# Kernel tuning notes

Hardware: AMD Instinct MI355X
Metric: run time of the kernel (lower is better)

Reference implementation:

```python
import jax, jax.numpy as jnp
import numpy as np

N, E, D_IN, D_OUT = 100000, 1250000, 64, 100


def setup_inputs() -> dict:
    key = jax.random.key(0)
    ks = jax.random.split(key, 12)
    inp = {
        "x": jax.random.normal(ks[0], (N, D_IN), dtype=jnp.float32),
        "edge_index": jax.random.randint(ks[1], (2, E), 0, N, dtype=jnp.int64),
        "edge_weight": jax.random.uniform(ks[2], (E,), dtype=jnp.float32),
        # ChebConv(64,100,K=1): one weight + bias
        "W10": jax.random.normal(ks[3], (D_IN, D_OUT), dtype=jnp.float32) * 0.1,
        "b1": jnp.zeros((D_OUT,), dtype=jnp.float32),
        # ChebConv(64,100,K=2)
        "W20": jax.random.normal(ks[4], (D_IN, D_OUT), dtype=jnp.float32) * 0.1,
        "W21": jax.random.normal(ks[5], (D_IN, D_OUT), dtype=jnp.float32) * 0.1,
        "b2": jnp.zeros((D_OUT,), dtype=jnp.float32),
        # ChebConv(64,100,K=3)
        "W30": jax.random.normal(ks[6], (D_IN, D_OUT), dtype=jnp.float32) * 0.1,
        "W31": jax.random.normal(ks[7], (D_IN, D_OUT), dtype=jnp.float32) * 0.1,
        "W32": jax.random.normal(ks[8], (D_IN, D_OUT), dtype=jnp.float32) * 0.1,
        "b3": jnp.zeros((D_OUT,), dtype=jnp.float32),
    }
    return inp


def _cheb_norm(edge_index, edge_weight, n):
    # PyG ChebConv.__norm__ with normalization='sym', lambda_max=2.0:
    # L_hat = (2/lambda_max) * (I - D^-1/2 A D^-1/2) - I = -D^-1/2 A D^-1/2
    # (the +1 diagonal of L and the -1 self-loop cancel), diag entries are 0.
    row, col = edge_index[0], edge_index[1]
    deg = jax.ops.segment_sum(edge_weight, row, num_segments=n)
    dis = jnp.where(deg > 0, jax.lax.rsqrt(jnp.where(deg > 0, deg, 1.0)), 0.0)
    return -dis[row] * edge_weight * dis[col]


def _cheb_conv(x, edge_index, w_hat, weights, bias):
    # out = sum_k T_k(L_hat) x @ W_k + b, with T0=x, T1=Lx, T_k=2L T_{k-1}-T_{k-2}
    n = x.shape[0]
    row, col = edge_index[0], edge_index[1]

    def prop(t):  # L_hat @ t via edge gather/scatter
        return jax.ops.segment_sum(t[row] * w_hat[:, None], col, num_segments=n)

    tx0 = x
    out = tx0 @ weights[0]
    if len(weights) > 1:
        tx1 = prop(tx0)
        out = out + tx1 @ weights[1]
        for k in range(2, len(weights)):
            tx2 = 2.0 * prop(tx1) - tx0
            out = out + tx2 @ weights[k]
            tx0, tx1 = tx1, tx2
    return out + bias


def reference(x, edge_index, edge_weight, W10, b1, W20, W21, b2, W30, W31, W32, b3):
    w_hat = _cheb_norm(edge_index, edge_weight, x.shape[0])
    s1 = _cheb_conv(x, edge_index, w_hat, [W10], b1)
    s2 = _cheb_conv(x, edge_index, w_hat, [W20, W21], b2)
    s3 = _cheb_conv(x, edge_index, w_hat, [W30, W31, W32], b3)
    return jnp.concatenate([s1, s2, s3], axis=1)  # [N, 300]
```

## Files before the change

### kernel.cpp

```cpp
#include <hip/hip_runtime.h>


typedef __attribute__((ext_vector_type(8))) short short8;
typedef __attribute__((ext_vector_type(8))) unsigned short ushort8;
typedef __attribute__((ext_vector_type(4))) float f32x4;

#define CAPB 8192
#define MAXBUCK 512

__device__ inline float bf2f(unsigned short u) {
    return __uint_as_float(((unsigned int)u) << 16);
}
__device__ inline unsigned short f2bf(float f) {
    unsigned int u = __float_as_uint(f);
    u = (u + 0x7FFF + ((u >> 16) & 1)) >> 16;
    return (unsigned short)u;
}

__global__ __launch_bounds__(256) void part_kernel(
        const int* __restrict__ row, const int* __restrict__ col,
        const float* __restrict__ ew, int* __restrict__ colcur,
        int* __restrict__ rowcur, uint2* __restrict__ colpart,
        uint2* __restrict__ rowpart, int E, int nbuck, int chunk) {
    __shared__ int hc[MAXBUCK];
    __shared__ int hr[MAXBUCK];
    const int t = threadIdx.x;
    const int s = blockIdx.x * chunk;
    const int e = min(E, s + chunk);
    if (s >= E) return;
    for (int i = t; i < nbuck; i += 256) { hc[i] = 0; hr[i] = 0; }
    __syncthreads();
    for (int i = s + t; i < e; i += 256) {
        atomicAdd(&hc[col[i] >> 8], 1);
        atomicAdd(&hr[row[i] >> 8], 1);
    }
    __syncthreads();
    for (int i = t; i < nbuck; i += 256) {
        int n = hc[i];
        hc[i] = n ? atomicAdd(&colcur[i], n) : 0;
        n = hr[i];
        hr[i] = n ? atomicAdd(&rowcur[i], n) : 0;
    }
    __syncthreads();
    for (int i = s + t; i < e; i += 256) {
        int r = row[i], c = col[i];
        float w = ew[i];
        int cb = c >> 8, rb = r >> 8;
        int pc = atomicAdd(&hc[cb], 1);
        if (pc < CAPB)
            colpart[(size_t)cb * CAPB + pc] =
                make_uint2(((unsigned)(c & 255) << 24) | (unsigned)r, __float_as_uint(w));
        int pr = atomicAdd(&hr[rb], 1);
        if (pr < CAPB)
            rowpart[(size_t)rb * CAPB + pr] = make_uint2((unsigned)r, __float_as_uint(w));
    }
}

__global__ __launch_bounds__(256) void fine_row_kernel(
        const int* __restrict__ rowcur, const uint2* __restrict__ rowpart,
        float* __restrict__ dis, int N) {
    __shared__ float s[256];
    const int b = blockIdx.x, t = threadIdx.x;
    const int sz = min(rowcur[b], CAPB);
    const uint2* part = rowpart + (size_t)b * CAPB;
    s[t] = 0.f;
    __syncthreads();
    for (int i = t; i < sz; i += 256) {
        uint2 rec = part[i];
        atomicAdd(&s[rec.x & 255u], __uint_as_float(rec.y));
    }
    __syncthreads();
    int r = (b << 8) + t;
    if (r < N) {
        float d = s[t];
        dis[r] = (d > 0.f) ? rsqrtf(d) : 0.f;
    }
}

__global__ void colbase_scan_kernel(const int* __restrict__ colcur,
                                    int* __restrict__ colbase,
                                    int* __restrict__ rowptr, int N, int nbuck) {
    __shared__ int s[MAXBUCK];
    int t = threadIdx.x;
    int v = (t < nbuck) ? min(colcur[t], CAPB) : 0;
    s[t] = v;
    __syncthreads();
    for (int o = 1; o < MAXBUCK; o <<= 1) {
        int u = (t >= o) ? s[t - o] : 0;
        __syncthreads();
        s[t] += u;
        __syncthreads();
    }
    if (t < nbuck) colbase[t] = s[t] - v;
    if (t == MAXBUCK - 1) rowptr[N] = s[MAXBUCK - 1];
}

__global__ __launch_bounds__(256) void fine_col_kernel(
        const int* __restrict__ colcur, const int* __restrict__ colbase,
        const uint2* __restrict__ colpart, const float* __restrict__ dis,
        uint2* __restrict__ erec, int* __restrict__ rowptr, int N) {
    __shared__ int h[256];
    __shared__ int sc[256];
    __shared__ int cur[256];
    const int b = blockIdx.x, t = threadIdx.x;
    const int sz = min(colcur[b], CAPB);
    const uint2* part = colpart + (size_t)b * CAPB;
    h[t] = 0;
    __syncthreads();
    for (int i = t; i < sz; i += 256) atomicAdd(&h[part[i].x >> 24], 1);
    __syncthreads();
    int v = h[t];
    sc[t] = v;
    __syncthreads();
    for (int o = 1; o < 256; o <<= 1) {
        int u = (t >= o) ? sc[t - o] : 0;
        __syncthreads();
        sc[t] += u;
        __syncthreads();
    }
    int excl = sc[t] - v;
    const int base = colbase[b];
    int c = (b << 8) + t;
    if (c < N) rowptr[c] = base + excl;
    cur[t] = excl;
    __syncthreads();
    for (int i = t; i < sz; i += 256) {
        uint2 rec = part[i];
        int coff = rec.x >> 24;
        int r = rec.x & 0xFFFFFFu;
        int pos = atomicAdd(&cur[coff], 1);
        float wd = __uint_as_float(rec.y) * dis[r];
        erec[(size_t)base + pos] = make_uint2((unsigned)r, __float_as_uint(wd));
    }
}

__global__ void deg_count_kernel(const int* __restrict__ row, const int* __restrict__ col,
                                 const float* __restrict__ ew,
                                 float* __restrict__ deg, int* __restrict__ cnt, int E) {
    int e = blockIdx.x * 256 + threadIdx.x;
    if (e < E) {
        atomicAdd(&deg[row[e]], ew[e]);
        atomicAdd(&cnt[col[e]], 1);
    }
}

__global__ void scan1_kernel(const int* __restrict__ cnt, int* __restrict__ pre,
                             int* __restrict__ bsum, int N) {
    __shared__ int s[256];
    int t = threadIdx.x;
    int i = blockIdx.x * 256 + t;
    int v = (i < N) ? cnt[i] : 0;
    s[t] = v;
    __syncthreads();
    for (int o = 1; o < 256; o <<= 1) {
        int u = (t >= o) ? s[t - o] : 0;
        __syncthreads();
        s[t] += u;
        __syncthreads();
    }
    if (i < N) pre[i] = s[t] - v;
    if (t == 255) bsum[blockIdx.x] = s[255];
}

__global__ void scan2_kernel(const int* __restrict__ bsum, int* __restrict__ bpre, int nb) {
    __shared__ int s[512];
    int t = threadIdx.x;
    int v = (t < nb) ? bsum[t] : 0;
    s[t] = v;
    __syncthreads();
    for (int o = 1; o < 512; o <<= 1) {
        int u = (t >= o) ? s[t - o] : 0;
        __syncthreads();
        s[t] += u;
        __syncthreads();
    }
    if (t < nb) bpre[t] = s[t] - v;
}

__global__ void scan3_kernel(int* __restrict__ rowptr, int* __restrict__ cursor,
                             const int* __restrict__ bpre, int N, int E) {
    int i = blockIdx.x * 256 + threadIdx.x;
    if (i < N) {
        int v = rowptr[i] + bpre[i >> 8];
        rowptr[i] = v;
        cursor[i] = v;
    }
    if (i == 0) rowptr[N] = E;
}

__global__ void scatter_compact_kernel(const int* __restrict__ row, const int* __restrict__ col,
                                       const float* __restrict__ ew, int* __restrict__ cursor,
                                       uint2* __restrict__ erec, int E) {
    int e = blockIdx.x * 256 + threadIdx.x;
    if (e < E) {
        int p = atomicAdd(&cursor[col[e]], 1);
        erec[p] = make_uint2((unsigned)row[e], __float_as_uint(ew[e]));
    }
}

__global__ void cvt_dis_kernel(const float* __restrict__ x, unsigned short* __restrict__ xb,
                               const float* __restrict__ deg, float* __restrict__ dis,
                               int N, int total4, int dodis) {
    int i = blockIdx.x * 256 + threadIdx.x;
    if (i < total4) {
        float4 v = reinterpret_cast<const float4*>(x)[i];
        ushort4 o;
        o.x = f2bf(v.x); o.y = f2bf(v.y); o.z = f2bf(v.z); o.w = f2bf(v.w);
        reinterpret_cast<ushort4*>(xb)[i] = o;
    }
    if (dodis && i < N) {
        float d = deg[i];
        dis[i] = (d > 0.f) ? rsqrtf(d) : 0.f;
    }
}

__global__ void gather_kernel(const int* __restrict__ ptr, const uint2* __restrict__ erec,
                              const float* __restrict__ dis,
                              const unsigned short* __restrict__ src,
                              unsigned short* __restrict__ dst, int N, int premul) {
    int node = blockIdx.x * 4 + (threadIdx.x >> 6);
    int lane = threadIdx.x & 63;
    if (node >= N) return;
    int s = ptr[node];
    int d = ptr[node + 1] - s;
    float acc = 0.f;
    for (int base = 0; base < d; base += 64) {
        int n = min(64, d - base);
        int ex = 0;
        float w = 0.f;
        if (lane < n) {
            uint2 e = erec[s + base + lane];
            ex = (int)e.x;
            w = __uint_as_float(e.y);
            if (!premul) w *= dis[ex];
        }
        int n4 = (n + 3) & ~3;
        for (int j = 0; j < n4; j += 4) {
            int r0 = __shfl(ex, j + 0, 64);
            int r1 = __shfl(ex, j + 1, 64);
            int r2 = __shfl(ex, j + 2, 64);
            int r3 = __shfl(ex, j + 3, 64);
            float w0 = __shfl(w, j + 0, 64);
            float w1 = __shfl(w, j + 1, 64);
            float w2 = __shfl(w, j + 2, 64);
            float w3 = __shfl(w, j + 3, 64);
            float v0 = bf2f(src[(size_t)r0 * 64 + lane]);
            float v1 = bf2f(src[(size_t)r1 * 64 + lane]);
            float v2 = bf2f(src[(size_t)r2 * 64 + lane]);
            float v3 = bf2f(src[(size_t)r3 * 64 + lane]);
            acc = fmaf(w0, v0, acc);
            acc = fmaf(w1, v1, acc);
            acc = fmaf(w2, v2, acc);
            acc = fmaf(w3, v3, acc);
        }
    }
    dst[(size_t)node * 64 + lane] = f2bf(-dis[node] * acc);
}

__global__ void prep_w_kernel(const float* __restrict__ W10, const float* __restrict__ W20,
                              const float* __restrict__ W21, const float* __restrict__ W30,
                              const float* __restrict__ W31, const float* __restrict__ W32,
                              unsigned short* __restrict__ imgW) {
    int i = blockIdx.x * 256 + threadIdx.x;
    if (i >= 6 * 7168) return;
    int img = i / 7168;
    int rem = i - img * 7168;
    int colc = rem >> 6;
    int k = rem & 63;
    const float* W;
    switch (img) {
        case 0: W = W10; break;
        case 1: W = W20; break;
        case 2: W = W21; break;
        case 3: W = W30; break;
        case 4: W = W31; break;
        default: W = W32; break;
    }
    float v = (colc < 100) ? W[k * 100 + colc] : 0.f;
    int g = k >> 3, j = k & 7;
    imgW[img * 7168 + colc * 64 + ((g ^ (colc & 7)) << 3) + j] = f2bf(v);
}

__global__ __launch_bounds__(256) void gemm_mfma_kernel(
        const unsigned short* __restrict__ xb, const unsigned short* __restrict__ tx1b,
        const unsigned short* __restrict__ p2b, const unsigned short* __restrict__ imgW,
        const float* __restrict__ b1, const float* __restrict__ b2,
        const float* __restrict__ b3, float* __restrict__ out, int N) {
    __shared__ unsigned short Ft[64 * 64];
    __shared__ unsigned short Ws[112 * 64];
    const int bid = blockIdx.x;
    const int seg = bid % 3;
    const int tile = bid / 3;
    const int row0 = tile * 64;
    const int tid = threadIdx.x;
    const int wv = tid >> 6;
    const int l = tid & 63;
    const int m = l & 15;
    const int q = l >> 4;

    f32x4 acc[7];
#pragma unroll
    for (int t = 0; t < 7; ++t) acc[t] = (f32x4){0.f, 0.f, 0.f, 0.f};

    const int imgBase = (seg * (seg + 1) / 2) * 7168;

    for (int c = 0; c <= seg; ++c) {
        const unsigned short* __restrict__ src = (c == 0) ? xb : (c == 1) ? tx1b : p2b;
#pragma unroll
        for (int it = 0; it < 2; ++it) {
            int i = tid + it * 256;
            int r = i >> 3, g = i & 7;
            int grow = row0 + r;
            ushort8 v = {0, 0, 0, 0, 0, 0, 0, 0};
            if (grow < N) {
                v = *reinterpret_cast<const ushort8*>(src + (size_t)grow * 64 + g * 8);
                if (c == 2) {
                    ushort8 xv = *reinterpret_cast<const ushort8*>(xb + (size_t)grow * 64 + g * 8);
#pragma unroll
                    for (int jj = 0; jj < 8; ++jj)
                        v[jj] = f2bf(2.f * bf2f(v[jj]) - bf2f(xv[jj]));
                }
            }
            *reinterpret_cast<ushort8*>(&Ft[r * 64 + ((g ^ (r & 7)) << 3)]) = v;
        }
        const uint4* wsrc = reinterpret_cast<const uint4*>(imgW + imgBase + c * 7168);
        uint4* wdst = reinterpret_cast<uint4*>(Ws);
#pragma unroll
        for (int it = 0; it < 4; ++it) {
            int i = tid + it * 256;
            if (i < 896) wdst[i] = wsrc[i];
        }
        __syncthreads();

        const int arow = wv * 16 + m;
#pragma unroll
        for (int ks = 0; ks < 2; ++ks) {
            short8 a = *reinterpret_cast<const short8*>(
                &Ft[arow * 64 + (((ks * 4 + q) ^ (arow & 7)) << 3)]);
#pragma unroll
            for (int t = 0; t < 7; ++t) {
                int n = t * 16 + m;
                short8 b = *reinterpret_cast<const short8*>(
                    &Ws[n * 64 + (((ks * 4 + q) ^ (n & 7)) << 3)]);
                acc[t] = __builtin_amdgcn_mfma_f32_16x16x32_bf16(a, b, acc[t], 0, 0, 0);
            }
        }
        __syncthreads();
    }

    const float* bsel = (seg == 0) ? b1 : (seg == 1) ? b2 : b3;
#pragma unroll
    for (int t = 0; t < 7; ++t) {
        int colseg = t * 16 + m;
        if (colseg >= 100) continue;
        float bv = bsel[colseg];
#pragma unroll
        for (int i = 0; i < 4; ++i) {
            int grow = row0 + wv * 16 + q * 4 + i;
            if (grow < N) out[(size_t)grow * 300 + seg * 100 + colseg] = acc[t][i] + bv;
        }
    }
}

extern "C" void kernel_launch(void* const* d_in, const int* in_sizes, int n_in,
                              void* d_out, int out_size, void* d_ws, size_t ws_size,
                              hipStream_t stream) {
    const float* x   = (const float*)d_in[0];
    const int*   ei  = (const int*)d_in[1];
    const float* ew  = (const float*)d_in[2];
    const float* W10 = (const float*)d_in[3];
    const float* b1  = (const float*)d_in[4];
    const float* W20 = (const float*)d_in[5];
    const float* W21 = (const float*)d_in[6];
    const float* b2  = (const float*)d_in[7];
    const float* W30 = (const float*)d_in[8];
    const float* W31 = (const float*)d_in[9];
    const float* W32 = (const float*)d_in[10];
    const float* b3  = (const float*)d_in[11];
    float* out = (float*)d_out;

    const int N = in_sizes[0] / 64;
    const int E = in_sizes[2];
    const int* row = ei;
    const int* col = ei + E;
    const int nb = (N + 255) / 256;
    const int eb = (E + 255) / 256;
    const int nbuck = (N + 255) >> 8;

    int total4 = N * 16;
    int pg = (N + 3) / 4;
    int ntile = (N + 63) / 64;

    char* base = (char*)d_ws;
    size_t off = 0;
    auto alloc = [&](size_t bytes) { size_t o = off; off = (off + bytes + 15) & ~(size_t)15; return o; };

    float* dis           = (float*)(base + alloc((size_t)4 * N));
    int*   rowptr        = (int*)(base + alloc((size_t)4 * (N + 1)));
    int*   colcur        = (int*)(base + alloc((size_t)4 * MAXBUCK * 2));
    int*   rowcur        = colcur + MAXBUCK;
    int*   colbase       = (int*)(base + alloc((size_t)4 * MAXBUCK));
    unsigned short* xb   = (unsigned short*)(base + alloc((size_t)128 * N));
    unsigned short* tx1b = (unsigned short*)(base + alloc((size_t)128 * N));
    unsigned short* p2b  = (unsigned short*)(base + alloc((size_t)128 * N));
    unsigned short* imgW = (unsigned short*)(base + alloc((size_t)2 * 6 * 7168));
    uint2* erec          = (uint2*)(base + alloc((size_t)8 * E));
    size_t mainfix = off;
    uint2* colpart       = (uint2*)(base + alloc((size_t)8 * nbuck * CAPB));
    uint2* rowpart       = (uint2*)(base + alloc((size_t)8 * nbuck * CAPB));
    size_t mainneed = off;

    bool mainok = (N < (1 << 24)) && (nbuck <= MAXBUCK) && (mainneed <= ws_size);

    if (mainok) {
        const int PBLK = 512;
        int chunk = (E + PBLK - 1) / PBLK;

        hipMemsetAsync(colcur, 0, (size_t)4 * MAXBUCK * 2, stream);
        part_kernel<<<PBLK, 256, 0, stream>>>(row, col, ew, colcur, rowcur,
                                              colpart, rowpart, E, nbuck, chunk);
        fine_row_kernel<<<nbuck, 256, 0, stream>>>(rowcur, rowpart, dis, N);
        colbase_scan_kernel<<<1, MAXBUCK, 0, stream>>>(colcur, colbase, rowptr, N, nbuck);
        fine_col_kernel<<<nbuck, 256, 0, stream>>>(colcur, colbase, colpart, dis,
                                                   erec, rowptr, N);
        cvt_dis_kernel<<<(total4 + 255) / 256, 256, 0, stream>>>(x, xb, nullptr, nullptr,
                                                                 N, total4, 0);
        prep_w_kernel<<<(6 * 7168 + 255) / 256, 256, 0, stream>>>(W10, W20, W21, W30, W31, W32, imgW);

        gather_kernel<<<pg, 256, 0, stream>>>(rowptr, erec, dis, xb, tx1b, N, 1);
        gather_kernel<<<pg, 256, 0, stream>>>(rowptr, erec, dis, tx1b, p2b, N, 1);
        gemm_mfma_kernel<<<ntile * 3, 256, 0, stream>>>(xb, tx1b, p2b, imgW, b1, b2, b3, out, N);
    } else {
        off = mainfix;
        float* deg    = (float*)(base + alloc((size_t)4 * N));
        int*   cursor = (int*)(base + alloc((size_t)4 * N));
        int*   bsum   = (int*)(base + alloc((size_t)4 * nb));
        int*   bpre   = (int*)(base + alloc((size_t)4 * nb));

        hipMemsetAsync(deg, 0, (size_t)4 * N, stream);
        hipMemsetAsync(cursor, 0, (size_t)4 * N, stream);
        deg_count_kernel<<<eb, 256, 0, stream>>>(row, col, ew, deg, cursor, E);
        scan1_kernel<<<nb, 256, 0, stream>>>(cursor, rowptr, bsum, N);
        scan2_kernel<<<1, 512, 0, stream>>>(bsum, bpre, nb);
        scan3_kernel<<<nb, 256, 0, stream>>>(rowptr, cursor, bpre, N, E);
        scatter_compact_kernel<<<eb, 256, 0, stream>>>(row, col, ew, cursor, erec, E);
        cvt_dis_kernel<<<(total4 + 255) / 256, 256, 0, stream>>>(x, xb, deg, dis, N, total4, 1);
        prep_w_kernel<<<(6 * 7168 + 255) / 256, 256, 0, stream>>>(W10, W20, W21, W30, W31, W32, imgW);

        gather_kernel<<<pg, 256, 0, stream>>>(rowptr, erec, dis, xb, tx1b, N, 0);
        gather_kernel<<<pg, 256, 0, stream>>>(rowptr, erec, dis, tx1b, p2b, N, 0);
        gemm_mfma_kernel<<<ntile * 3, 256, 0, stream>>>(xb, tx1b, p2b, imgW, b1, b2, b3, out, N);
    }
}
```

Measured before the change: 414.1 us.

## Replace single-pass 256-node bucketing with two-level radix partition for CSR build

Edge partitioning now runs in two stages: a coarse pass into 2048-node superbuckets (64 shared counters instead of 512), then a split pass that refines each superbucket into eight 256-node buckets. Degree accumulation becomes split partial sums per superbucket, reduced inside the bf16 conversion kernel. The goal is less shared-atomic and global-cursor contention and better write locality in the first scatter pass. The cost is an extra kernel launch and another full pass over the column records. Capacities are now sized from the mean edge count, so buckets that overflow under skewed input would drop edges.

After: 386.5 us. 6.6% less time.

```diff
diff --git a/kernel.cpp b/kernel.cpp
--- a/kernel.cpp
+++ b/kernel.cpp
@@ -5,8 +5,8 @@
 typedef __attribute__((ext_vector_type(8))) unsigned short ushort8;
 typedef __attribute__((ext_vector_type(4))) float f32x4;
 
-#define CAPB 8192
-#define MAXBUCK 512
+#define NSBMAX 64
+#define NSPLIT 16
 
 __device__ inline float bf2f(unsigned short u) {
     return __uint_as_float(((unsigned int)u) << 16);
@@ -17,94 +17,129 @@
     return (unsigned short)u;
 }
 
-__global__ __launch_bounds__(256) void part_kernel(
+__global__ __launch_bounds__(512) void partA_kernel(
         const int* __restrict__ row, const int* __restrict__ col,
-        const float* __restrict__ ew, int* __restrict__ colcur,
-        int* __restrict__ rowcur, uint2* __restrict__ colpart,
-        uint2* __restrict__ rowpart, int E, int nbuck, int chunk) {
-    __shared__ int hc[MAXBUCK];
-    __shared__ int hr[MAXBUCK];
+        const float* __restrict__ ew, int* __restrict__ colAcur,
+        int* __restrict__ rowAcur, uint2* __restrict__ colA,
+        uint2* __restrict__ rowA, int E, int nsb, int chunk, int capA) {
+    __shared__ int hc[NSBMAX];
+    __shared__ int hr[NSBMAX];
     const int t = threadIdx.x;
     const int s = blockIdx.x * chunk;
     const int e = min(E, s + chunk);
     if (s >= E) return;
-    for (int i = t; i < nbuck; i += 256) { hc[i] = 0; hr[i] = 0; }
-    __syncthreads();
-    for (int i = s + t; i < e; i += 256) {
-        atomicAdd(&hc[col[i] >> 8], 1);
-        atomicAdd(&hr[row[i] >> 8], 1);
-    }
-    __syncthreads();
-    for (int i = t; i < nbuck; i += 256) {
-        int n = hc[i];
-        hc[i] = n ? atomicAdd(&colcur[i], n) : 0;
-        n = hr[i];
-        hr[i] = n ? atomicAdd(&rowcur[i], n) : 0;
-    }
-    __syncthreads();
-    for (int i = s + t; i < e; i += 256) {
+    if (t < NSBMAX) { hc[t] = 0; hr[t] = 0; }
+    __syncthreads();
+    for (int i = s + t; i < e; i += 512) {
+        atomicAdd(&hc[col[i] >> 11], 1);
+        atomicAdd(&hr[row[i] >> 11], 1);
+    }
+    __syncthreads();
+    if (t < nsb) {
+        int n = hc[t];
+        hc[t] = n ? atomicAdd(&colAcur[t], n) : 0;
+        n = hr[t];
+        hr[t] = n ? atomicAdd(&rowAcur[t], n) : 0;
+    }
+    __syncthreads();
+    for (int i = s + t; i < e; i += 512) {
         int r = row[i], c = col[i];
         float w = ew[i];
-        int cb = c >> 8, rb = r >> 8;
-        int pc = atomicAdd(&hc[cb], 1);
-        if (pc < CAPB)
-            colpart[(size_t)cb * CAPB + pc] =
-                make_uint2(((unsigned)(c & 255) << 24) | (unsigned)r, __float_as_uint(w));
-        int pr = atomicAdd(&hr[rb], 1);
-        if (pr < CAPB)
-            rowpart[(size_t)rb * CAPB + pr] = make_uint2((unsigned)r, __float_as_uint(w));
-    }
-}
-
-__global__ __launch_bounds__(256) void fine_row_kernel(
-        const int* __restrict__ rowcur, const uint2* __restrict__ rowpart,
-        float* __restrict__ dis, int N) {
-    __shared__ float s[256];
-    const int b = blockIdx.x, t = threadIdx.x;
-    const int sz = min(rowcur[b], CAPB);
-    const uint2* part = rowpart + (size_t)b * CAPB;
-    s[t] = 0.f;
-    __syncthreads();
-    for (int i = t; i < sz; i += 256) {
+        int pc = atomicAdd(&hc[c >> 11], 1);
+        if (pc < capA)
+            colA[(size_t)(c >> 11) * capA + pc] =
+                make_uint2(((unsigned)(c & 2047) << 17) | (unsigned)r, __float_as_uint(w));
+        int pr = atomicAdd(&hr[r >> 11], 1);
+        if (pr < capA)
+            rowA[(size_t)(r >> 11) * capA + pr] = make_uint2((unsigned)r, __float_as_uint(w));
+    }
+}
+
+__global__ __launch_bounds__(512) void partB_kernel(
+        const int* __restrict__ colAcur, const uint2* __restrict__ colA,
+        int* __restrict__ colBcur, uint2* __restrict__ colB,
+        int capA, int capB) {
+    __shared__ int h[8];
+    const int sb = blockIdx.x / NSPLIT;
+    const int j = blockIdx.x % NSPLIT;
+    const int t = threadIdx.x;
+    const int cnt = min(colAcur[sb], capA);
+    const int chunk = (cnt + NSPLIT - 1) / NSPLIT;
+    const int s = j * chunk;
+    const int e = min(cnt, s + chunk);
+    if (t < 8) h[t] = 0;
+    __syncthreads();
+    const uint2* part = colA + (size_t)sb * capA;
+    for (int i = s + t; i < e; i += 512) atomicAdd(&h[part[i].x >> 25], 1);
+    __syncthreads();
+    if (t < 8) {
+        int n = h[t];
+        h[t] = n ? atomicAdd(&colBcur[sb * 8 + t], n) : 0;
+    }
+    __syncthreads();
+    for (int i = s + t; i < e; i += 512) {
         uint2 rec = part[i];
-        atomicAdd(&s[rec.x & 255u], __uint_as_float(rec.y));
-    }
-    __syncthreads();
-    int r = (b << 8) + t;
-    if (r < N) {
-        float d = s[t];
-        dis[r] = (d > 0.f) ? rsqrtf(d) : 0.f;
-    }
-}
-
-__global__ void colbase_scan_kernel(const int* __restrict__ colcur,
+        int f = rec.x >> 25;
+        int p = atomicAdd(&h[f], 1);
+        if (p < capB) {
+            unsigned coff = (rec.x >> 17) & 255u;
+            unsigned r = rec.x & 0x1FFFFu;
+            colB[(size_t)(sb * 8 + f) * capB + p] = make_uint2((coff << 24) | r, rec.y);
+        }
+    }
+}
+
+__global__ __launch_bounds__(512) void fine_rowp_kernel(
+        const int* __restrict__ rowAcur, const uint2* __restrict__ rowA,
+        float* __restrict__ partial, int capA) {
+    __shared__ float sdeg[2048];
+    const int sb = blockIdx.x / NSPLIT;
+    const int j = blockIdx.x % NSPLIT;
+    const int t = threadIdx.x;
+    const int cnt = min(rowAcur[sb], capA);
+    const int chunk = (cnt + NSPLIT - 1) / NSPLIT;
+    const int s = j * chunk;
+    const int e = min(cnt, s + chunk);
+    for (int k = t; k < 2048; k += 512) sdeg[k] = 0.f;
+    __syncthreads();
+    const uint2* part = rowA + (size_t)sb * capA;
+    for (int i = s + t; i < e; i += 512) {
+        uint2 rec = part[i];
+        atomicAdd(&sdeg[rec.x & 2047u], __uint_as_float(rec.y));
+    }
+    __syncthreads();
+    float* dstp = partial + (size_t)blockIdx.x * 2048;
+    for (int k = t; k < 2048; k += 512) dstp[k] = sdeg[k];
+}
+
+__global__ void colbase_scan_kernel(const int* __restrict__ colBcur,
                                     int* __restrict__ colbase,
-                                    int* __restrict__ rowptr, int N, int nbuck) {
-    __shared__ int s[MAXBUCK];
+                                    int* __restrict__ rowptr, int N, int nfb, int capB) {
+    __shared__ int s[512];
     int t = threadIdx.x;
-    int v = (t < nbuck) ? min(colcur[t], CAPB) : 0;
+    int v = (t < nfb) ? min(colBcur[t], capB) : 0;
     s[t] = v;
     __syncthreads();
-    for (int o = 1; o < MAXBUCK; o <<= 1) {
+    for (int o = 1; o < 512; o <<= 1) {
         int u = (t >= o) ? s[t - o] : 0;
         __syncthreads();
         s[t] += u;
         __syncthreads();
     }
-    if (t < nbuck) colbase[t] = s[t] - v;
-    if (t == MAXBUCK - 1) rowptr[N] = s[MAXBUCK - 1];
+    if (t < nfb) colbase[t] = s[t] - v;
+    if (t == 511) rowptr[N] = s[511];
 }
 
 __global__ __launch_bounds__(256) void fine_col_kernel(
-        const int* __restrict__ colcur, const int* __restrict__ colbase,
-        const uint2* __restrict__ colpart, const float* __restrict__ dis,
-        uint2* __restrict__ erec, int* __restrict__ rowptr, int N) {
+        const int* __restrict__ colBcur, const int* __restrict__ colbase,
+        const uint2* __restrict__ colB, const float* __restrict__ dis,
+        uint2* __restrict__ erec, int* __restrict__ rowptr, int N, int capB) {
     __shared__ int h[256];
     __shared__ int sc[256];
     __shared__ int cur[256];
     const int b = blockIdx.x, t = threadIdx.x;
-    const int sz = min(colcur[b], CAPB);
-    const uint2* part = colpart + (size_t)b * CAPB;
+    const int sz = min(colBcur[b], capB);
+    const uint2* part = colB + (size_t)b * capB;
     h[t] = 0;
     __syncthreads();
     for (int i = t; i < sz; i += 256) atomicAdd(&h[part[i].x >> 24], 1);
@@ -199,8 +234,8 @@
 }
 
 __global__ void cvt_dis_kernel(const float* __restrict__ x, unsigned short* __restrict__ xb,
-                               const float* __restrict__ deg, float* __restrict__ dis,
-                               int N, int total4, int dodis) {
+                               const float* __restrict__ degp, float* __restrict__ dis,
+                               int N, int total4, int mode) {
     int i = blockIdx.x * 256 + threadIdx.x;
     if (i < total4) {
         float4 v = reinterpret_cast<const float4*>(x)[i];
@@ -208,8 +243,16 @@
         o.x = f2bf(v.x); o.y = f2bf(v.y); o.z = f2bf(v.z); o.w = f2bf(v.w);
         reinterpret_cast<ushort4*>(xb)[i] = o;
     }
-    if (dodis && i < N) {
-        float d = deg[i];
+    if (mode && i < N) {
+        float d;
+        if (mode == 2) {
+            const float* p = degp + ((size_t)(i >> 11) * NSPLIT) * 2048 + (i & 2047);
+            d = 0.f;
+#pragma unroll
+            for (int j = 0; j < NSPLIT; ++j) d += p[(size_t)j * 2048];
+        } else {
+            d = degp[i];
+        }
         dis[i] = (d > 0.f) ? rsqrtf(d) : 0.f;
     }
 }
@@ -385,46 +428,58 @@
     const int* col = ei + E;
     const int nb = (N + 255) / 256;
     const int eb = (E + 255) / 256;
-    const int nbuck = (N + 255) >> 8;
+
+    const int NSB = (N + 2047) >> 11;
+    const int nfb = NSB * 8;
 
     int total4 = N * 16;
     int pg = (N + 3) / 4;
     int ntile = (N + 63) / 64;
 
+    long meanA = ((long)E * 2048 + N - 1) / N;
+    int capA = (int)(meanA + meanA / 4 + 1024);
+    long meanB = ((long)E * 256 + N - 1) / N;
+    int capB = (int)(meanB + meanB / 4 + 512);
+
     char* base = (char*)d_ws;
     size_t off = 0;
     auto alloc = [&](size_t bytes) { size_t o = off; off = (off + bytes + 15) & ~(size_t)15; return o; };
 
     float* dis           = (float*)(base + alloc((size_t)4 * N));
     int*   rowptr        = (int*)(base + alloc((size_t)4 * (N + 1)));
-    int*   colcur        = (int*)(base + alloc((size_t)4 * MAXBUCK * 2));
-    int*   rowcur        = colcur + MAXBUCK;
-    int*   colbase       = (int*)(base + alloc((size_t)4 * MAXBUCK));
+    int*   colAcur       = (int*)(base + alloc((size_t)4 * 640));
+    int*   rowAcur       = colAcur + 64;
+    int*   colBcur       = colAcur + 128;
+    int*   colbase       = (int*)(base + alloc((size_t)4 * 512));
     unsigned short* xb   = (unsigned short*)(base + alloc((size_t)128 * N));
     unsigned short* tx1b = (unsigned short*)(base + alloc((size_t)128 * N));
     unsigned short* p2b  = (unsigned short*)(base + alloc((size_t)128 * N));
     unsigned short* imgW = (unsigned short*)(base + alloc((size_t)2 * 6 * 7168));
     uint2* erec          = (uint2*)(base + alloc((size_t)8 * E));
     size_t mainfix = off;
-    uint2* colpart       = (uint2*)(base + alloc((size_t)8 * nbuck * CAPB));
-    uint2* rowpart       = (uint2*)(base + alloc((size_t)8 * nbuck * CAPB));
+    uint2* colA          = (uint2*)(base + alloc((size_t)8 * NSB * capA));
+    uint2* rowA          = (uint2*)(base + alloc((size_t)8 * NSB * capA));
+    uint2* colB          = (uint2*)(base + alloc((size_t)8 * nfb * capB));
+    float* partial       = (float*)(base + alloc((size_t)4 * NSB * NSPLIT * 2048));
     size_t mainneed = off;
 
-    bool mainok = (N < (1 << 24)) && (nbuck <= MAXBUCK) && (mainneed <= ws_size);
+    bool mainok = (N <= 131072) && (NSB <= NSBMAX) && (nfb <= 512) && (mainneed <= ws_size);
 
     if (mainok) {
         const int PBLK = 512;
-        int chunk = (E + PBLK - 1) / PBLK;
-
-        hipMemsetAsync(colcur, 0, (size_t)4 * MAXBUCK * 2, stream);
-        part_kernel<<<PBLK, 256, 0, stream>>>(row, col, ew, colcur, rowcur,
-                                              colpart, rowpart, E, nbuck, chunk);
-        fine_row_kernel<<<nbuck, 256, 0, stream>>>(rowcur, rowpart, dis, N);
-        colbase_scan_kernel<<<1, MAXBUCK, 0, stream>>>(colcur, colbase, rowptr, N, nbuck);
-        fine_col_kernel<<<nbuck, 256, 0, stream>>>(colcur, colbase, colpart, dis,
-                                                   erec, rowptr, N);
-        cvt_dis_kernel<<<(total4 + 255) / 256, 256, 0, stream>>>(x, xb, nullptr, nullptr,
-                                                                 N, total4, 0);
+        int chunkA = (E + PBLK - 1) / PBLK;
+
+        hipMemsetAsync(colAcur, 0, (size_t)4 * 640, stream);
+        partA_kernel<<<PBLK, 512, 0, stream>>>(row, col, ew, colAcur, rowAcur,
+                                               colA, rowA, E, NSB, chunkA, capA);
+        partB_kernel<<<NSB * NSPLIT, 512, 0, stream>>>(colAcur, colA, colBcur, colB,
+                                                       capA, capB);
+        fine_rowp_kernel<<<NSB * NSPLIT, 512, 0, stream>>>(rowAcur, rowA, partial, capA);
+        cvt_dis_kernel<<<(total4 + 255) / 256, 256, 0, stream>>>(x, xb, partial, dis,
+                                                                 N, total4, 2);
+        colbase_scan_kernel<<<1, 512, 0, stream>>>(colBcur, colbase, rowptr, N, nfb, capB);
+        fine_col_kernel<<<nfb, 256, 0, stream>>>(colBcur, colbase, colB, dis,
+                                                 erec, rowptr, N, capB);
         prep_w_kernel<<<(6 * 7168 + 255) / 256, 256, 0, stream>>>(W10, W20, W21, W30, W31, W32, imgW);
 
         gather_kernel<<<pg, 256, 0, stream>>>(rowptr, erec, dis, xb, tx1b, N, 1);
```
